# Kernel tuning notes

Hardware: AMD Instinct MI355X
Metric: run time of the kernel (lower is better)

Reference implementation:

```python
import jax, jax.numpy as jnp
import numpy as np

EPS_LOG = 1e-8
EPS_CHECK = 1e-4


def to_float8(x, exp_bits=4, mant_bits=3):
    # fp8 emulation: sign/abs/log2/floor/clamp/round chain
    max_exp = 2 ** (exp_bits - 1) - 1
    min_exp = -max_exp
    scale = 2.0 ** mant_bits
    sign = jnp.sign(x)
    x_abs = jnp.abs(x)
    exp = jnp.clip(jnp.floor(jnp.log2(x_abs + EPS_LOG)), min_exp, max_exp)
    pow2 = jnp.exp2(exp)
    mant = x_abs / pow2 - 1.0
    mant_q = jnp.round(mant * scale) / scale
    return sign * (1.0 + mant_q) * pow2


def checksum_verify(left, right, epsilon=EPS_CHECK):
    # ABFT: augment left with a column-sum row, right with a row-sum column
    left_cs = jnp.concatenate([left, jnp.sum(left, axis=0, keepdims=True)], axis=0)
    right_cs = jnp.concatenate([right, jnp.sum(right, axis=1, keepdims=True)], axis=1)
    prod_cs = left_cs @ right_cs  # [(m+1), (n+1)]
    output = prod_cs[:-1, :-1]
    row_sum_check = prod_cs[:-1, -1]
    col_sum_check = prod_cs[-1, :-1]
    col_diff = jnp.abs(jnp.sum(output, axis=0) - col_sum_check)
    row_diff = jnp.abs(jnp.sum(output, axis=1) - row_sum_check)
    mask = (row_diff > epsilon)[:, None] & (col_diff > epsilon)[None, :]
    return output, mask


def setup_inputs() -> dict:
    key = jax.random.key(0)
    kx, ku, kA, kB, kC = jax.random.split(key, 5)
    batch, n, m, p = 4096, 2048, 1024, 1024
    return {
        "x": jax.random.normal(kx, (batch, n), dtype=jnp.float32),
        "u": jax.random.normal(ku, (batch, m), dtype=jnp.float32),
        "A": jax.random.normal(kA, (n, n), dtype=jnp.float32),
        "B": jax.random.normal(kB, (n, m), dtype=jnp.float32),
        "C": jax.random.normal(kC, (p, n), dtype=jnp.float32),
    }


def reference(x, u, A, B, C):
    int_bits, frac_bits = 4, 3
    Aq = to_float8(A, int_bits, frac_bits)
    Bq = to_float8(B, int_bits, frac_bits)
    left_term, left_mask = checksum_verify(x, Aq.T)
    right_term, right_mask = checksum_verify(u, Bq.T)
    x_next = to_float8(left_term + right_term, int_bits, frac_bits)
    _ = left_mask | right_mask  # mask computed but discarded in forward (as in torch)
    Cq = to_float8(C, int_bits, frac_bits)
    y = to_float8(x_next @ Cq.T, int_bits, frac_bits)
    return (x_next, y)
```

## Files before the change

### kernel.cpp

```cpp
#include <hip/hip_runtime.h>
#include <hip/hip_bf16.h>
#include <stdint.h>

typedef __bf16 bf16_t;
typedef __attribute__((ext_vector_type(8))) __bf16 bf16x8;
typedef __attribute__((ext_vector_type(4))) float f32x4;

__device__ __forceinline__ float q8(float v) {
    float a = __builtin_fabsf(v);
    float z = a + 1e-8f;
    int ei = ((__float_as_int(z) >> 23) & 0xff) - 127;
    ei = ei > 7 ? 7 : (ei < -7 ? -7 : ei);
    float p  = __int_as_float((ei + 127) << 23);
    float ip = __int_as_float((127 - ei) << 23);
    float m  = __builtin_fmaf(a, ip, -1.0f);
    float mq = __builtin_rintf(m * 8.0f) * 0.125f;
    float r  = (1.0f + mq) * p;
    return v < 0.0f ? -r : r;
}

__device__ __forceinline__ void gload_lds16(const bf16_t* g, bf16_t* l) {
    __builtin_amdgcn_global_load_lds(
        (__attribute__((address_space(1))) void*)(g),
        (__attribute__((address_space(3))) void*)(l), 16, 0, 0);
}

__device__ __forceinline__ bf16x8 cvt8(float4 a, float4 b) {
    bf16x8 o = { (bf16_t)a.x, (bf16_t)a.y, (bf16_t)a.z, (bf16_t)a.w,
                 (bf16_t)b.x, (bf16_t)b.y, (bf16_t)b.z, (bf16_t)b.w };
    return o;
}
__device__ __forceinline__ bf16x8 q8x8(float4 a, float4 b) {
    bf16x8 o = { (bf16_t)q8(a.x), (bf16_t)q8(a.y), (bf16_t)q8(a.z), (bf16_t)q8(a.w),
                 (bf16_t)q8(b.x), (bf16_t)q8(b.y), (bf16_t)q8(b.z), (bf16_t)q8(b.w) };
    return o;
}

__global__ void pack_all(const float* __restrict__ x, const float* __restrict__ u,
                         const float* __restrict__ A, const float* __restrict__ B,
                         const float* __restrict__ C,
                         bf16_t* __restrict__ XU, bf16_t* __restrict__ AB,
                         bf16_t* __restrict__ CQ) {
    const unsigned bid = blockIdx.x;
    const int tid = threadIdx.x;
    if (bid < 4096u) {
        size_t r = bid; int col = tid * 8;
        float4 v0 = *(const float4*)&x[r * 2048 + col];
        float4 v1 = *(const float4*)&x[r * 2048 + col + 4];
        *(bf16x8*)&XU[r * 3072 + col] = cvt8(v0, v1);
    } else if (bid < 6144u) {
        unsigned b = bid - 4096u;
        size_t r = b * 2 + (tid >> 7); int col = (tid & 127) * 8;
        float4 v0 = *(const float4*)&u[r * 1024 + col];
        float4 v1 = *(const float4*)&u[r * 1024 + col + 4];
        *(bf16x8*)&XU[r * 3072 + 2048 + col] = cvt8(v0, v1);
    } else if (bid < 8192u) {
        size_t r = bid - 6144u; int col = tid * 8;
        float4 v0 = *(const float4*)&A[r * 2048 + col];
        float4 v1 = *(const float4*)&A[r * 2048 + col + 4];
        *(bf16x8*)&AB[r * 3072 + col] = q8x8(v0, v1);
    } else if (bid < 9216u) {
        unsigned b = bid - 8192u;
        size_t r = b * 2 + (tid >> 7); int col = (tid & 127) * 8;
        float4 v0 = *(const float4*)&B[r * 1024 + col];
        float4 v1 = *(const float4*)&B[r * 1024 + col + 4];
        *(bf16x8*)&AB[r * 3072 + 2048 + col] = q8x8(v0, v1);
    } else {
        size_t r = bid - 9216u; int col = tid * 8;
        float4 v0 = *(const float4*)&C[r * 2048 + col];
        float4 v1 = *(const float4*)&C[r * 2048 + col + 4];
        *(bf16x8*)&CQ[r * 2048 + col] = q8x8(v0, v1);
    }
}

template<int BN, bool DUAL>
__global__ __launch_bounds__(256, (BN == 128) ? 2 : 3)
void gemm_q8_v6(const bf16_t* __restrict__ A, const bf16_t* __restrict__ B,
                float* __restrict__ outf, bf16_t* __restrict__ outb,
                int N, int K) {
    constexpr int BM = 128;
    constexpr int BK = 128;
    constexpr int NI = BN / 32;
    constexpr int A_ITS = BM * (BK / 8) / 256;
    constexpr int B_ITS = BN * (BK / 8) / 256;

    __shared__ alignas(16) bf16_t sA[BM * BK];
    __shared__ alignas(16) bf16_t sB[BN * BK];

    const int tid  = threadIdx.x;
    const int lane = tid & 63;
    const int wave = tid >> 6;
    const int wm   = wave & 1;
    const int wn   = wave >> 1;
    const int ln16 = lane & 15;
    const int quad = lane >> 4;

    const int b   = blockIdx.x;
    const int xcd = b & 7;
    const int g   = b >> 3;
    const int bx  = (xcd & 1) * 8 + (g & 7);
    const int by  = (xcd >> 1) * 8 + (g >> 3);
    const int brow = by * BM;
    const int bcol = bx * BN;

    const int srow = tid >> 4;
    const int scol = ((tid & 15) ^ srow) * 8;
    const bf16_t* gA0 = A + (size_t)(brow + srow) * K + scol;
    const bf16_t* gB0 = B + (size_t)(bcol + srow) * K + scol;

    int a_off[4][4], b_off[NI][4];
#pragma unroll
    for (int im = 0; im < 4; ++im) {
        int r = wm * 64 + im * 16 + ln16;
#pragma unroll
        for (int s = 0; s < 4; ++s) {
            int cg = s * 4 + quad;
            a_off[im][s] = (r * 16 + (cg ^ (r & 15))) * 8;
        }
    }
#pragma unroll
    for (int in = 0; in < NI; ++in) {
        int r = wn * (BN / 2) + in * 16 + ln16;
#pragma unroll
        for (int s = 0; s < 4; ++s) {
            int cg = s * 4 + quad;
            b_off[in][s] = (r * 16 + (cg ^ (r & 15))) * 8;
        }
    }

    f32x4 acc[4][NI];
#pragma unroll
    for (int im = 0; im < 4; ++im)
#pragma unroll
        for (int in = 0; in < NI; ++in)
            acc[im][in] = (f32x4){0.f, 0.f, 0.f, 0.f};

    for (int kt = 0; kt < K; kt += BK) {
#pragma unroll
        for (int it = 0; it < A_ITS; ++it)
            gload_lds16(gA0 + (size_t)it * 16 * K, sA + it * 2048 + wave * 512);
        gA0 += BK;
#pragma unroll
        for (int it = 0; it < B_ITS; ++it)
            gload_lds16(gB0 + (size_t)it * 16 * K, sB + it * 2048 + wave * 512);
        gB0 += BK;
        __syncthreads();
#pragma unroll
        for (int s = 0; s < 4; ++s) {
            bf16x8 af[4], bfv[NI];
#pragma unroll
            for (int im = 0; im < 4; ++im) af[im]  = *(const bf16x8*)(sA + a_off[im][s]);
#pragma unroll
            for (int in = 0; in < NI; ++in) bfv[in] = *(const bf16x8*)(sB + b_off[in][s]);
#pragma unroll
            for (int im = 0; im < 4; ++im)
#pragma unroll
                for (int in = 0; in < NI; ++in)
                    acc[im][in] = __builtin_amdgcn_mfma_f32_16x16x32_bf16(
                        af[im], bfv[in], acc[im][in], 0, 0, 0);
        }
        __syncthreads();
    }

    const int rbase = quad * 4;
#pragma unroll
    for (int im = 0; im < 4; ++im) {
#pragma unroll
        for (int in = 0; in < NI; ++in) {
            int gm = brow + wm * 64 + im * 16 + rbase;
            int gn = bcol + wn * (BN / 2) + in * 16 + ln16;
#pragma unroll
            for (int r = 0; r < 4; ++r) {
                float v = q8(acc[im][in][r]);
                outf[(size_t)(gm + r) * N + gn] = v;
                if (DUAL) outb[(size_t)(gm + r) * N + gn] = (bf16_t)v;
            }
        }
    }
}

extern "C" void kernel_launch(void* const* d_in, const int* in_sizes, int n_in,
                              void* d_out, int out_size, void* d_ws, size_t ws_size,
                              hipStream_t stream) {
    const float* x = (const float*)d_in[0];
    const float* u = (const float*)d_in[1];
    const float* A = (const float*)d_in[2];
    const float* B = (const float*)d_in[3];
    const float* C = (const float*)d_in[4];

    float* outf = (float*)d_out;
    float* xnf  = outf;
    float* yf   = outf + (size_t)4096 * 2048;

    uint8_t* ws = (uint8_t*)d_ws;
    bf16_t* XU = (bf16_t*)ws;
    bf16_t* AB = (bf16_t*)(ws + (size_t)25165824);
    bf16_t* CQ = (bf16_t*)(ws + (size_t)25165824 + 12582912);
    bf16_t* XN = (bf16_t*)(ws + (size_t)25165824 + 12582912 + 4194304);

    pack_all<<<dim3(10240), 256, 0, stream>>>(x, u, A, B, C, XU, AB, CQ);

    gemm_q8_v6<128, true><<<dim3(512), 256, 0, stream>>>(
        XU, AB, xnf, XN, 2048, 3072);
    gemm_q8_v6<64, false><<<dim3(512), 256, 0, stream>>>(
        XN, CQ, yf, nullptr, 1024, 2048);
}
```

Before: 199.8 us.

## Fuse pack and both GEMMs into one persistent kernel with grid barriers

```diff
diff --git a/kernel.cpp b/kernel.cpp
--- a/kernel.cpp
+++ b/kernel.cpp
@@ -36,56 +36,36 @@
     return o;
 }
 
-__global__ void pack_all(const float* __restrict__ x, const float* __restrict__ u,
-                         const float* __restrict__ A, const float* __restrict__ B,
-                         const float* __restrict__ C,
-                         bf16_t* __restrict__ XU, bf16_t* __restrict__ AB,
-                         bf16_t* __restrict__ CQ) {
-    const unsigned bid = blockIdx.x;
-    const int tid = threadIdx.x;
-    if (bid < 4096u) {
-        size_t r = bid; int col = tid * 8;
-        float4 v0 = *(const float4*)&x[r * 2048 + col];
-        float4 v1 = *(const float4*)&x[r * 2048 + col + 4];
-        *(bf16x8*)&XU[r * 3072 + col] = cvt8(v0, v1);
-    } else if (bid < 6144u) {
-        unsigned b = bid - 4096u;
-        size_t r = b * 2 + (tid >> 7); int col = (tid & 127) * 8;
-        float4 v0 = *(const float4*)&u[r * 1024 + col];
-        float4 v1 = *(const float4*)&u[r * 1024 + col + 4];
-        *(bf16x8*)&XU[r * 3072 + 2048 + col] = cvt8(v0, v1);
-    } else if (bid < 8192u) {
-        size_t r = bid - 6144u; int col = tid * 8;
-        float4 v0 = *(const float4*)&A[r * 2048 + col];
-        float4 v1 = *(const float4*)&A[r * 2048 + col + 4];
-        *(bf16x8*)&AB[r * 3072 + col] = q8x8(v0, v1);
-    } else if (bid < 9216u) {
-        unsigned b = bid - 8192u;
-        size_t r = b * 2 + (tid >> 7); int col = (tid & 127) * 8;
-        float4 v0 = *(const float4*)&B[r * 1024 + col];
-        float4 v1 = *(const float4*)&B[r * 1024 + col + 4];
-        *(bf16x8*)&AB[r * 3072 + 2048 + col] = q8x8(v0, v1);
-    } else {
-        size_t r = bid - 9216u; int col = tid * 8;
-        float4 v0 = *(const float4*)&C[r * 2048 + col];
-        float4 v1 = *(const float4*)&C[r * 2048 + col + 4];
-        *(bf16x8*)&CQ[r * 2048 + col] = q8x8(v0, v1);
-    }
+__device__ __forceinline__ void grid_barrier(unsigned int* ctr, unsigned int target) {
+    __syncthreads();
+    if (threadIdx.x == 0) {
+        __threadfence();
+        atomicAdd(ctr, 1u);
+        int guard = 0;
+        while (__hip_atomic_load(ctr, __ATOMIC_RELAXED, __HIP_MEMORY_SCOPE_AGENT)
+                   < target && guard < (1 << 22)) {
+            __builtin_amdgcn_s_sleep(8);
+            ++guard;
+        }
+        __threadfence();
+    }
+    __syncthreads();
 }
 
 template<int BN, bool DUAL>
-__global__ __launch_bounds__(256, (BN == 128) ? 2 : 3)
-void gemm_q8_v6(const bf16_t* __restrict__ A, const bf16_t* __restrict__ B,
-                float* __restrict__ outf, bf16_t* __restrict__ outb,
-                int N, int K) {
+__device__ __forceinline__ void gemm_body(const bf16_t* __restrict__ A,
+                                          const bf16_t* __restrict__ B,
+                                          float* __restrict__ outf,
+                                          bf16_t* __restrict__ outb,
+                                          int N, int K, bf16_t* smem) {
     constexpr int BM = 128;
     constexpr int BK = 128;
     constexpr int NI = BN / 32;
     constexpr int A_ITS = BM * (BK / 8) / 256;
     constexpr int B_ITS = BN * (BK / 8) / 256;
 
-    __shared__ alignas(16) bf16_t sA[BM * BK];
-    __shared__ alignas(16) bf16_t sB[BN * BK];
+    bf16_t* sA = smem;
+    bf16_t* sB = smem + BM * BK;
 
     const int tid  = threadIdx.x;
     const int lane = tid & 63;
@@ -177,6 +157,61 @@
             }
         }
     }
+}
+
+__global__ __launch_bounds__(256, 2)
+void fused_all(const float* __restrict__ x, const float* __restrict__ u,
+               const float* __restrict__ A, const float* __restrict__ B,
+               const float* __restrict__ C,
+               bf16_t* __restrict__ XU, bf16_t* __restrict__ AB,
+               bf16_t* __restrict__ CQ, bf16_t* __restrict__ XN,
+               float* __restrict__ xnf, float* __restrict__ yf,
+               unsigned int* __restrict__ bar) {
+    __shared__ alignas(16) bf16_t smem[32768];
+
+    {
+        const int gid = blockIdx.x * 256 + threadIdx.x;
+#pragma unroll 1
+        for (int i = gid; i < 2621440; i += 131072) {
+            if (i < 1048576) {
+                int r = i >> 8, c = (i & 255) * 8;
+                float4 v0 = *(const float4*)&x[(size_t)r * 2048 + c];
+                float4 v1 = *(const float4*)&x[(size_t)r * 2048 + c + 4];
+                *(bf16x8*)&XU[(size_t)r * 3072 + c] = cvt8(v0, v1);
+            } else if (i < 1572864) {
+                int j = i - 1048576;
+                int r = j >> 7, c = (j & 127) * 8;
+                float4 v0 = *(const float4*)&u[(size_t)r * 1024 + c];
+                float4 v1 = *(const float4*)&u[(size_t)r * 1024 + c + 4];
+                *(bf16x8*)&XU[(size_t)r * 3072 + 2048 + c] = cvt8(v0, v1);
+            } else if (i < 2097152) {
+                int j = i - 1572864;
+                int r = j >> 8, c = (j & 255) * 8;
+                float4 v0 = *(const float4*)&A[(size_t)r * 2048 + c];
+                float4 v1 = *(const float4*)&A[(size_t)r * 2048 + c + 4];
+                *(bf16x8*)&AB[(size_t)r * 3072 + c] = q8x8(v0, v1);
+            } else if (i < 2359296) {
+                int j = i - 2097152;
+                int r = j >> 7, c = (j & 127) * 8;
+                float4 v0 = *(const float4*)&B[(size_t)r * 1024 + c];
+                float4 v1 = *(const float4*)&B[(size_t)r * 1024 + c + 4];
+                *(bf16x8*)&AB[(size_t)r * 3072 + 2048 + c] = q8x8(v0, v1);
+            } else {
+                int j = i - 2359296;
+                int r = j >> 8, c = (j & 255) * 8;
+                float4 v0 = *(const float4*)&C[(size_t)r * 2048 + c];
+                float4 v1 = *(const float4*)&C[(size_t)r * 2048 + c + 4];
+                *(bf16x8*)&CQ[(size_t)r * 2048 + c] = q8x8(v0, v1);
+            }
+        }
+    }
+    grid_barrier(bar + 0, 512u);
+
+    gemm_body<128, true>(XU, AB, xnf, XN, 2048, 3072, smem);
+
+    grid_barrier(bar + 16, 512u);
+
+    gemm_body<64, false>(XN, CQ, yf, nullptr, 1024, 2048, smem);
 }
 
 extern "C" void kernel_launch(void* const* d_in, const int* in_sizes, int n_in,
@@ -197,11 +232,10 @@
     bf16_t* AB = (bf16_t*)(ws + (size_t)25165824);
     bf16_t* CQ = (bf16_t*)(ws + (size_t)25165824 + 12582912);
     bf16_t* XN = (bf16_t*)(ws + (size_t)25165824 + 12582912 + 4194304);
-
-    pack_all<<<dim3(10240), 256, 0, stream>>>(x, u, A, B, C, XU, AB, CQ);
-
-    gemm_q8_v6<128, true><<<dim3(512), 256, 0, stream>>>(
-        XU, AB, xnf, XN, 2048, 3072);
-    gemm_q8_v6<64, false><<<dim3(512), 256, 0, stream>>>(
-        XN, CQ, yf, nullptr, 1024, 2048);
-}
+    size_t bar_off = (ws_size - 128) & ~(size_t)63;
+    unsigned int* bar = (unsigned int*)(ws + bar_off);
+
+    hipMemsetAsync(bar, 0, 128, stream);
+    fused_all<<<dim3(512), dim3(256), 0, stream>>>(
+        x, u, A, B, C, XU, AB, CQ, XN, xnf, yf, bar);
+}
```

After: 319.0 us. 59.7% more time.

## Add triple-buffered 256x128 GEMM kernel with phased loads for first GEMM

Applied to the files above, without the earlier changes.

```diff
diff --git a/kernel.cpp b/kernel.cpp
--- a/kernel.cpp
+++ b/kernel.cpp
@@ -73,13 +73,177 @@
     }
 }
 
-template<int BN, bool DUAL>
-__global__ __launch_bounds__(256, (BN == 128) ? 2 : 3)
+__global__ __launch_bounds__(512, 1)
+void gemm1_8ph(const bf16_t* __restrict__ Ap, const bf16_t* __restrict__ Bp,
+               float* __restrict__ outf, bf16_t* __restrict__ outb,
+               int N, int K) {
+    constexpr int BM = 256;
+    constexpr int BN = 128;
+    constexpr int BK = 64;
+
+    __shared__ alignas(16) bf16_t sA[3][BM * BK];
+    __shared__ alignas(16) bf16_t sB[3][BN * BK];
+
+    const int tid  = threadIdx.x;
+    const int lane = tid & 63;
+    const int wave = tid >> 6;
+    const int wm   = wave & 3;
+    const int wn   = wave >> 2;
+    const int ln16 = lane & 15;
+    const int quad = lane >> 4;
+
+    const int b   = blockIdx.x;
+    const int xcd = b & 7;
+    const int g   = b >> 3;
+    const int bx  = (xcd & 1) * 8 + (g & 7);
+    const int by  = (xcd >> 1) * 4 + (g >> 3);
+    const int brow = by * BM;
+    const int bcol = bx * BN;
+
+    const bf16_t* gA[4];
+#pragma unroll
+    for (int it = 0; it < 4; ++it) {
+        int L = it * 512 + tid;
+        int r = L >> 3, c = L & 7;
+        gA[it] = Ap + (size_t)(brow + r) * K + (c ^ (r & 7)) * 8;
+    }
+    const bf16_t* gB[2];
+#pragma unroll
+    for (int it = 0; it < 2; ++it) {
+        int L = it * 512 + tid;
+        int r = L >> 3, c = L & 7;
+        gB[it] = Bp + (size_t)(bcol + r) * K + (c ^ (r & 7)) * 8;
+    }
+
+    int a_off[4][2], b_off[2][2][2];
+#pragma unroll
+    for (int im = 0; im < 4; ++im) {
+        int r = wm * 64 + im * 16 + ln16;
+#pragma unroll
+        for (int s = 0; s < 2; ++s) {
+            int cg = s * 4 + quad;
+            a_off[im][s] = (r * 8 + (cg ^ (r & 7))) * 8;
+        }
+    }
+#pragma unroll
+    for (int nq = 0; nq < 2; ++nq)
+#pragma unroll
+        for (int in = 0; in < 2; ++in) {
+            int r = wn * 64 + nq * 32 + in * 16 + ln16;
+#pragma unroll
+            for (int s = 0; s < 2; ++s) {
+                int cg = s * 4 + quad;
+                b_off[nq][in][s] = (r * 8 + (cg ^ (r & 7))) * 8;
+            }
+        }
+
+    f32x4 acc[4][4];
+#pragma unroll
+    for (int im = 0; im < 4; ++im)
+#pragma unroll
+        for (int jn = 0; jn < 4; ++jn)
+            acc[im][jn] = (f32x4){0.f, 0.f, 0.f, 0.f};
+
+    auto STAGE_HALF = [&](int sb, int h) {
+        gload_lds16(gA[2 * h],     &sA[sb][((2 * h) * 512 + wave * 64) * 8]);
+        gA[2 * h] += BK;
+        gload_lds16(gA[2 * h + 1], &sA[sb][((2 * h + 1) * 512 + wave * 64) * 8]);
+        gA[2 * h + 1] += BK;
+        gload_lds16(gB[h],         &sB[sb][(h * 512 + wave * 64) * 8]);
+        gB[h] += BK;
+    };
+
+    STAGE_HALF(0, 0); STAGE_HALF(0, 1);
+    STAGE_HALF(1, 0); STAGE_HALF(1, 1);
+    asm volatile("s_waitcnt vmcnt(6)" ::: "memory");
+    __builtin_amdgcn_s_barrier();
+    asm volatile("" ::: "memory");
+
+    const int NT = K / BK;
+    for (int t = 0; t < NT; ++t) {
+        const int rb = t % 3;
+        int sb = rb + 2; if (sb >= 3) sb -= 3;
+        const bool st = (t + 2 < NT);
+        const bf16_t* bA = sA[rb];
+        const bf16_t* bB = sB[rb];
+
+        bf16x8 afr[4][2], bfr[2][2];
+
+#pragma unroll
+        for (int im = 0; im < 4; ++im) {
+            afr[im][0] = *(const bf16x8*)(bA + a_off[im][0]);
+            afr[im][1] = *(const bf16x8*)(bA + a_off[im][1]);
+        }
+#pragma unroll
+        for (int in = 0; in < 2; ++in) {
+            bfr[in][0] = *(const bf16x8*)(bB + b_off[0][in][0]);
+            bfr[in][1] = *(const bf16x8*)(bB + b_off[0][in][1]);
+        }
+        if (st) STAGE_HALF(sb, 0);
+        __builtin_amdgcn_s_barrier();
+        asm volatile("s_waitcnt lgkmcnt(0)" ::: "memory");
+        __builtin_amdgcn_s_setprio(1);
+#pragma unroll
+        for (int s = 0; s < 2; ++s)
+#pragma unroll
+            for (int im = 0; im < 4; ++im)
+#pragma unroll
+                for (int in = 0; in < 2; ++in)
+                    acc[im][in] = __builtin_amdgcn_mfma_f32_16x16x32_bf16(
+                        afr[im][s], bfr[in][s], acc[im][in], 0, 0, 0);
+        __builtin_amdgcn_s_setprio(0);
+        __builtin_amdgcn_s_barrier();
+        asm volatile("" ::: "memory");
+
+#pragma unroll
+        for (int in = 0; in < 2; ++in) {
+            bfr[in][0] = *(const bf16x8*)(bB + b_off[1][in][0]);
+            bfr[in][1] = *(const bf16x8*)(bB + b_off[1][in][1]);
+        }
+        if (st) STAGE_HALF(sb, 1);
+        __builtin_amdgcn_s_barrier();
+        asm volatile("s_waitcnt lgkmcnt(0)" ::: "memory");
+        __builtin_amdgcn_s_setprio(1);
+#pragma unroll
+        for (int s = 0; s < 2; ++s)
+#pragma unroll
+            for (int im = 0; im < 4; ++im)
+#pragma unroll
+                for (int in = 0; in < 2; ++in)
+                    acc[im][2 + in] = __builtin_amdgcn_mfma_f32_16x16x32_bf16(
+                        afr[im][s], bfr[in][s], acc[im][2 + in], 0, 0, 0);
+        __builtin_amdgcn_s_setprio(0);
+        if (st) asm volatile("s_waitcnt vmcnt(6)" ::: "memory");
+        else    asm volatile("s_waitcnt vmcnt(0)" ::: "memory");
+        __builtin_amdgcn_s_barrier();
+        asm volatile("" ::: "memory");
+    }
+
+    const int rbase = quad * 4;
+#pragma unroll
+    for (int im = 0; im < 4; ++im) {
+#pragma unroll
+        for (int nq = 0; nq < 2; ++nq)
+#pragma unroll
+            for (int in = 0; in < 2; ++in) {
+                int gm = brow + wm * 64 + im * 16 + rbase;
+                int gn = bcol + wn * 64 + nq * 32 + in * 16 + ln16;
+#pragma unroll
+                for (int r = 0; r < 4; ++r) {
+                    float v = q8(acc[im][nq * 2 + in][r]);
+                    outf[(size_t)(gm + r) * N + gn] = v;
+                    outb[(size_t)(gm + r) * N + gn] = (bf16_t)v;
+                }
+            }
+    }
+}
+
+__global__ __launch_bounds__(256, 3)
 void gemm_q8_v6(const bf16_t* __restrict__ A, const bf16_t* __restrict__ B,
-                float* __restrict__ outf, bf16_t* __restrict__ outb,
-                int N, int K) {
+                float* __restrict__ outf, int N, int K) {
     constexpr int BM = 128;
     constexpr int BK = 128;
+    constexpr int BN = 64;
     constexpr int NI = BN / 32;
     constexpr int A_ITS = BM * (BK / 8) / 256;
     constexpr int B_ITS = BN * (BK / 8) / 256;
@@ -170,11 +334,8 @@
             int gm = brow + wm * 64 + im * 16 + rbase;
             int gn = bcol + wn * (BN / 2) + in * 16 + ln16;
 #pragma unroll
-            for (int r = 0; r < 4; ++r) {
-                float v = q8(acc[im][in][r]);
-                outf[(size_t)(gm + r) * N + gn] = v;
-                if (DUAL) outb[(size_t)(gm + r) * N + gn] = (bf16_t)v;
-            }
+            for (int r = 0; r < 4; ++r)
+                outf[(size_t)(gm + r) * N + gn] = q8(acc[im][in][r]);
         }
     }
 }
@@ -200,8 +361,6 @@
 
     pack_all<<<dim3(10240), 256, 0, stream>>>(x, u, A, B, C, XU, AB, CQ);
 
-    gemm_q8_v6<128, true><<<dim3(512), 256, 0, stream>>>(
-        XU, AB, xnf, XN, 2048, 3072);
-    gemm_q8_v6<64, false><<<dim3(512), 256, 0, stream>>>(
-        XN, CQ, yf, nullptr, 1024, 2048);
-}
+    gemm1_8ph<<<dim3(256), 512, 0, stream>>>(XU, AB, xnf, XN, 2048, 3072);
+    gemm_q8_v6<<<dim3(512), 256, 0, stream>>>(XN, CQ, yf, 1024, 2048);
+}
```

Result: slower. 209.9 us (+5.1%).
